# Optimization experiments

Hardware: AMD Instinct MI355X
Metric: run time of the kernel (lower is better)

Reference implementation:

```python
import jax, jax.numpy as jnp
import numpy as np

N = 100000   # nodes
E = 1600000  # edges (avg degree 16)
D = 64       # feature dim
LN_EPS = 1e-5


def setup_inputs() -> dict:
    key = jax.random.key(0)
    ks = jax.random.split(key, 12)
    s = 1.0 / np.sqrt(D)
    x = jax.random.normal(ks[0], (N, D), dtype=jnp.float32)
    edge_index = jax.random.randint(ks[1], (2, E), 0, N, dtype=jnp.int32)
    routing_factor = jax.random.uniform(ks[2], (E,), dtype=jnp.float32)
    return {
        "x": x,
        "edge_index": edge_index,
        "routing_factor": routing_factor,
        "W_phys": jax.random.normal(ks[3], (D, D), dtype=jnp.float32) * s,
        "W_neur": jax.random.normal(ks[4], (D, D), dtype=jnp.float32) * s,
        "att_w": jax.random.normal(ks[5], (2 * D,), dtype=jnp.float32) * s,
        "channel_fusion": jnp.float32(0.5),
        "mlp_w1": jax.random.normal(ks[6], (2 * D, D), dtype=jnp.float32) * s,
        "mlp_b1": jnp.zeros((2 * D,), dtype=jnp.float32),
        "mlp_w2": jax.random.normal(ks[7], (D, 2 * D), dtype=jnp.float32) / np.sqrt(2 * D),
        "mlp_b2": jnp.zeros((D,), dtype=jnp.float32),
        "ln1_g": jnp.ones((D,), dtype=jnp.float32),
        "ln1_b": jnp.zeros((D,), dtype=jnp.float32),
        "ln2_g": jnp.ones((D,), dtype=jnp.float32),
        "ln2_b": jnp.zeros((D,), dtype=jnp.float32),
    }


def _layernorm(h, g, b):
    mu = jnp.mean(h, axis=-1, keepdims=True)
    var = jnp.var(h, axis=-1, keepdims=True)
    return (h - mu) * jax.lax.rsqrt(var + LN_EPS) * g + b


def reference(x, edge_index, routing_factor, W_phys, W_neur, att_w,
              channel_fusion, mlp_w1, mlp_b1, mlp_w2, mlp_b2,
              ln1_g, ln1_b, ln2_g, ln2_b):
    src, dst = edge_index[0], edge_index[1]
    x_src = x[src]  # [E, D]
    # att(cat([x_src, x_dst])) == x_src @ w[:D] + x_dst @ w[D:]
    att_scores = x_src @ att_w[:D] + x[dst] @ att_w[D:]  # [E]
    # segment softmax over destination nodes (equivalent to per-node loop)
    seg_max = jax.ops.segment_max(att_scores, dst, num_segments=N)
    e = jnp.exp(att_scores - seg_max[dst])
    denom = jax.ops.segment_sum(e, dst, num_segments=N)
    att = e / denom[dst]  # [E]
    # dual-channel messages (dropout inactive at eval)
    phys = routing_factor[:, None] * (x_src @ W_phys.T)
    neur = x_src @ W_neur.T
    alpha = jax.nn.sigmoid(channel_fusion)
    messages = att[:, None] * (alpha * phys + (1.0 - alpha) * neur)  # [E, D]
    out = jax.ops.segment_sum(messages, dst, num_segments=N)  # [N, D]
    h = _layernorm(jax.nn.gelu(out, approximate=False) + x, ln1_g, ln1_b)
    m = jax.nn.gelu(h @ mlp_w1.T + mlp_b1, approximate=False) @ mlp_w2.T + mlp_b2
    return _layernorm(m + h, ln2_g, ln2_b)
```

## Files before the change

kernel.cpp:

```cpp
#include <hip/hip_runtime.h>
#include <math.h>

#define NN 100000
#define NE 1600000
#define DD 64
#define NBUK 782
#define TILE 2048
#define NTB ((NE + TILE - 1) / TILE)
#define BSTRIDE 3072
#define SCAP 3072

typedef __attribute__((ext_vector_type(8))) short short8;
typedef __attribute__((ext_vector_type(4))) float f32x4;
typedef __attribute__((ext_vector_type(4))) _Float16 h4;
typedef __attribute__((ext_vector_type(2))) _Float16 f16x2;

__device__ __forceinline__ float gelu_exact(float v) {
    return 0.5f * v * (1.0f + erff(v * 0.7071067811865475f));
}

__device__ __forceinline__ unsigned short f2bf(float f) {
    unsigned u = __float_as_uint(f);
    return (unsigned short)((u + 0x7FFFu + ((u >> 16) & 1u)) >> 16);
}
__device__ __forceinline__ float bf2f(unsigned short h) {
    return __uint_as_float((unsigned)h << 16);
}
__device__ __forceinline__ void split8v(float4 x0, float4 x1, short8& hi, short8& lo) {
    float v[8] = {x0.x, x0.y, x0.z, x0.w, x1.x, x1.y, x1.z, x1.w};
    #pragma unroll
    for (int i = 0; i < 8; ++i) {
        unsigned short h = f2bf(v[i]);
        hi[i] = (short)h;
        lo[i] = (short)f2bf(v[i] - bf2f(h));
    }
}
__device__ __forceinline__ void lds_frag(const float* g, int row, int u0, int s,
                                         short8& hi, short8& lo) {
    float4 p0 = *(const float4*)&g[row * 64 + ((u0 ^ s) << 2)];
    float4 p1 = *(const float4*)&g[row * 64 + (((u0 + 1) ^ s) << 2)];
    split8v(p0, p1, hi, lo);
}

__device__ __forceinline__ f16x2 as_f16x2(unsigned int u) {
    union { unsigned int x; f16x2 h; } c; c.x = u; return c.h;
}
__device__ __forceinline__ unsigned short h_as_us(_Float16 h) {
    union { _Float16 h; unsigned short u; } c; c.h = h; return c.u;
}
__device__ __forceinline__ float us_as_f(unsigned short u) {
    union { unsigned short u; _Float16 h; } c; c.u = u; return (float)c.h;
}

__global__ __launch_bounds__(256) void k01(
    const float* __restrict__ Wp, const float* __restrict__ Wn,
    const float* __restrict__ w1, const float* __restrict__ w2,
    const float* __restrict__ cf,
    unsigned short* __restrict__ wh, unsigned short* __restrict__ wl,
    const float* __restrict__ x, const float* __restrict__ attw,
    float* __restrict__ es1, _Float16* __restrict__ xh)
{
    int bid = blockIdx.x;
    if (bid < 96) {
        int t = bid * 256 + threadIdx.x;
        float alpha = 1.0f / (1.0f + __expf(-cf[0]));
        float beta  = 1.0f - alpha;
        float v;
        if (t < 8192) {
            int d = t >> 7, k = t & 127;
            v = (k < 64) ? alpha * Wp[d * 64 + k] : beta * Wn[d * 64 + (k - 64)];
        } else if (t < 16384) {
            v = w1[t - 8192];
        } else {
            v = w2[t - 16384];
        }
        unsigned short h = f2bf(v);
        wh[t] = h;
        wl[t] = f2bf(v - bf2f(h));
    } else {
        int n = (bid - 96) * 256 + threadIdx.x;
        if (n >= NN) return;
        const float4* x4 = (const float4*)(x + (size_t)n * DD);
        float a = 0.f;
        #pragma unroll
        for (int i = 0; i < DD/4; ++i) {
            float4 v = x4[i];
            a += v.x*attw[4*i+0] + v.y*attw[4*i+1] + v.z*attw[4*i+2] + v.w*attw[4*i+3];
            h4 hv = {(_Float16)v.x, (_Float16)v.y, (_Float16)v.z, (_Float16)v.w};
            *(h4*)(xh + (size_t)n * DD + 4*i) = hv;
        }
        es1[n] = __expf(a);
    }
}

__global__ __launch_bounds__(1024) void ks_bscan(
    const int* __restrict__ bcount, int* __restrict__ bbase)
{
    __shared__ int sa[1024], sb[1024];
    int t = threadIdx.x;
    int v = (t < NBUK) ? bcount[t] : 0;
    sa[t] = v;
    __syncthreads();
    int* s = sa; int* d = sb;
    #pragma unroll
    for (int o = 1; o < 1024; o <<= 1) {
        d[t] = s[t] + ((t >= o) ? s[t - o] : 0);
        __syncthreads();
        int* tmp = s; s = d; d = tmp;
    }
    if (t < NBUK) bbase[t] = s[t] - v;
    if (t == 0) bbase[NBUK] = NE;
}

__global__ __launch_bounds__(256) void kscat1(
    const int* __restrict__ ei, const float* __restrict__ rf,
    const float* __restrict__ es1,
    int* __restrict__ bcount, uint2* __restrict__ tmp)
{
    __shared__ int hist[NBUK];
    __shared__ int gbase[NBUK];
    for (int i = threadIdx.x; i < NBUK; i += 256) hist[i] = 0;
    __syncthreads();
    int base = blockIdx.x * TILE;
    int end  = min(base + TILE, NE);
    for (int e = base + threadIdx.x; e < end; e += 256)
        atomicAdd(&hist[ei[NE + e] >> 7], 1);
    __syncthreads();
    for (int i = threadIdx.x; i < NBUK; i += 256) {
        int c = hist[i];
        gbase[i] = c ? (i * BSTRIDE + atomicAdd(bcount + i, c)) : 0;
        hist[i] = 0;
    }
    __syncthreads();
    for (int e = base + threadIdx.x; e < end; e += 256) {
        int src = ei[e];
        int dst = ei[NE + e];
        float es = es1[src];
        float ef = es * rf[e];
        unsigned packed = (unsigned)h_as_us((_Float16)es)
                        | ((unsigned)h_as_us((_Float16)ef) << 16);
        int b = dst >> 7;
        int t = atomicAdd(&hist[b], 1);
        tmp[gbase[b] + t] =
            make_uint2((unsigned)src | ((unsigned)(dst & 127) << 17), packed);
    }
}

__global__ __launch_bounds__(256) void kscat2(
    const uint2* __restrict__ tmp, const int* __restrict__ bcount,
    const int* __restrict__ bbase,
    int* __restrict__ off, uint2* __restrict__ sorted)
{
    __shared__ int hist[128], scn[128], tick[128];
    __shared__ uint2 obuf[SCAP];
    int b   = blockIdx.x;
    int tid = threadIdx.x;
    int si = b * BSTRIDE;
    int so = bbase[b];
    int m  = bcount[b];

    if (tid < 128) { hist[tid] = 0; tick[tid] = 0; }
    __syncthreads();

    for (int i = tid; i < m; i += 256)
        atomicAdd(&hist[tmp[si + i].x >> 17], 1);
    __syncthreads();

    if (tid < 128) scn[tid] = hist[tid];
    __syncthreads();
    #pragma unroll
    for (int o = 1; o < 128; o <<= 1) {
        int v = (tid < 128 && tid >= o) ? scn[tid - o] : 0;
        __syncthreads();
        if (tid < 128) scn[tid] += v;
        __syncthreads();
    }

    int nb0 = b * 128;
    if (tid < 128 && nb0 + tid < NN) off[nb0 + tid] = so + scn[tid] - hist[tid];
    if (b == NBUK - 1 && tid == 0) off[NN] = NE;
    __syncthreads();

    for (int i = tid; i < m; i += 256) {
        uint2 pr = tmp[si + i];
        int l = pr.x >> 17;
        int t = atomicAdd(&tick[l], 1);
        int lp = (scn[l] - hist[l]) + t;
        uint2 val = make_uint2(pr.x & 0x1FFFFu, pr.y);
        if (lp < SCAP) obuf[lp] = val;
        else sorted[so + lp] = val;
    }
    __syncthreads();
    int mm = min(m, SCAP);
    for (int i = tid; i < mm; i += 256)
        sorted[so + i] = obuf[i];
}

__global__ __launch_bounds__(256) void k4a_agg(
    const uint2* __restrict__ sorted, const int* __restrict__ off,
    const _Float16* __restrict__ xh, float* __restrict__ uv)
{
    int lane = threadIdx.x & 63;
    int n = blockIdx.x * 4 + (threadIdx.x >> 6);
    int r0 = __builtin_amdgcn_readfirstlane(off[n]);
    int r1 = __builtin_amdgcn_readfirstlane(off[n + 1]);
    const unsigned short* xs = (const unsigned short*)xh;

    float den = 0.f, u = 0.f, v = 0.f;
    const unsigned ONES = 0x3C003C00u;
    int j = r0;
    for (; j + 8 <= r1; j += 8) {
        uint2 p[8];
        #pragma unroll
        for (int t = 0; t < 8; ++t) p[t] = sorted[j + t];
        unsigned xv[4];
        #pragma unroll
        for (int q = 0; q < 4; ++q) {
            unsigned a0 = xs[(size_t)p[2*q].x   * DD + lane];
            unsigned a1 = xs[(size_t)p[2*q+1].x * DD + lane];
            xv[q] = a0 | (a1 << 16);
        }
        #pragma unroll
        for (int q = 0; q < 4; ++q) {
            unsigned y0 = p[2*q].y, y1 = p[2*q+1].y;
            unsigned e2 = (y0 & 0xFFFFu) | (y1 << 16);
            unsigned f2 = (y0 >> 16) | (y1 & 0xFFFF0000u);
            v   = __builtin_amdgcn_fdot2(as_f16x2(xv[q]), as_f16x2(e2), v, false);
            u   = __builtin_amdgcn_fdot2(as_f16x2(xv[q]), as_f16x2(f2), u, false);
            den = __builtin_amdgcn_fdot2(as_f16x2(e2), as_f16x2(ONES), den, false);
        }
    }
    for (; j + 2 <= r1; j += 2) {
        uint2 p0 = sorted[j], p1 = sorted[j + 1];
        unsigned a0 = xs[(size_t)p0.x * DD + lane];
        unsigned a1 = xs[(size_t)p1.x * DD + lane];
        unsigned xv = a0 | (a1 << 16);
        unsigned e2 = (p0.y & 0xFFFFu) | (p1.y << 16);
        unsigned f2 = (p0.y >> 16) | (p1.y & 0xFFFF0000u);
        v   = __builtin_amdgcn_fdot2(as_f16x2(xv), as_f16x2(e2), v, false);
        u   = __builtin_amdgcn_fdot2(as_f16x2(xv), as_f16x2(f2), u, false);
        den = __builtin_amdgcn_fdot2(as_f16x2(e2), as_f16x2(ONES), den, false);
    }
    if (j < r1) {
        uint2 p0 = sorted[j];
        float xvf = us_as_f((unsigned short)xs[(size_t)p0.x * DD + lane]);
        float e = us_as_f((unsigned short)(p0.y & 0xFFFFu));
        float f = us_as_f((unsigned short)(p0.y >> 16));
        den += e; v += e * xvf; u += f * xvf;
    }
    float inv = (r1 > r0) ? 1.f / den : 0.f;
    uv[(size_t)n * 128 + lane]      = u * inv;
    uv[(size_t)n * 128 + 64 + lane] = v * inv;
}

__global__ __launch_bounds__(512, 4) void k4b5(
    const float* __restrict__ uv,
    const unsigned short* __restrict__ wh, const unsigned short* __restrict__ wl,
    const float* __restrict__ x,
    const float* __restrict__ g1, const float* __restrict__ be1,
    const float* __restrict__ bb1, const float* __restrict__ bb2,
    const float* __restrict__ g2, const float* __restrict__ be2,
    float* __restrict__ out)
{
    __shared__ unsigned short WH[8192], WL[8192];
    __shared__ unsigned short W2H[4096], W2L[4096];
    __shared__ float Gt[8][1024];

    int tid  = threadIdx.x;
    int lane = tid & 63;
    int wv   = tid >> 6;
    int quad = lane >> 4, l16 = lane & 15;
    int s7   = l16 & 7;
    int nb = blockIdx.x * 128 + wv * 16;
    float* gt = Gt[wv];

    const float4* arow4 = (const float4*)(uv + (size_t)min(nb + l16, NN - 1) * 128);
    float4 av[8];
    #pragma unroll
    for (int ks = 0; ks < 4; ++ks) {
        av[2*ks]   = arow4[ks*8 + quad*2];
        av[2*ks+1] = arow4[ks*8 + quad*2 + 1];
    }
    float xr[4][4];
    #pragma unroll
    for (int r = 0; r < 4; ++r) {
        size_t nld = (size_t)min(nb + quad*4 + r, NN - 1) * 64;
        #pragma unroll
        for (int nt = 0; nt < 4; ++nt) xr[r][nt] = x[nld + nt*16 + l16];
    }

    #pragma unroll
    for (int k = 0; k < 2; ++k) {
        int i = tid + k*512;
        int row = i >> 4, u = i & 15;
        int up = u ^ (row & 7);
        *(short8*)&WH[row*128 + up*8] = *(const short8*)&wh[i*8];
        *(short8*)&WL[row*128 + up*8] = *(const short8*)&wl[i*8];
    }
    __syncthreads();

    f32x4 acc0[4] = {};
    #pragma unroll
    for (int ks = 0; ks < 4; ++ks) {
        short8 ah, al;
        split8v(av[2*ks], av[2*ks+1], ah, al);
        int u0 = 4*ks + quad;
        #pragma unroll
        for (int nt = 0; nt < 4; ++nt) {
            int wo = (nt*16 + l16)*128 + (u0 ^ s7)*8;
            short8 bh = *(const short8*)&WH[wo];
            short8 bl = *(const short8*)&WL[wo];
            acc0[nt] = __builtin_amdgcn_mfma_f32_16x16x32_bf16(ah, bh, acc0[nt], 0, 0, 0);
            acc0[nt] = __builtin_amdgcn_mfma_f32_16x16x32_bf16(al, bh, acc0[nt], 0, 0, 0);
            acc0[nt] = __builtin_amdgcn_mfma_f32_16x16x32_bf16(ah, bl, acc0[nt], 0, 0, 0);
        }
    }

    float hn[4][4];
    #pragma unroll
    for (int r = 0; r < 4; ++r) {
        float hv[4];
        #pragma unroll
        for (int nt = 0; nt < 4; ++nt)
            hv[nt] = gelu_exact(acc0[nt][r]) + xr[r][nt];
        float s = hv[0] + hv[1] + hv[2] + hv[3];
        #pragma unroll
        for (int o = 1; o < 16; o <<= 1) s += __shfl_xor(s, o);
        float mu = s * (1.0f/64.0f);
        float q = 0.f;
        #pragma unroll
        for (int nt = 0; nt < 4; ++nt) { float t = hv[nt] - mu; q += t*t; }
        #pragma unroll
        for (int o = 1; o < 16; o <<= 1) q += __shfl_xor(q, o);
        float rs = rsqrtf(q * (1.0f/64.0f) + 1e-5f);
        int row = quad*4 + r;
        #pragma unroll
        for (int nt = 0; nt < 4; ++nt) {
            int c = nt*16 + l16;
            float h = (hv[nt] - mu) * rs * g1[c] + be1[c];
            hn[r][nt] = h;
            int u = c >> 2;
            gt[row*64 + ((u ^ (row & 7)) << 2) + (c & 3)] = h;
        }
    }
    __syncthreads();

    #pragma unroll
    for (int k = 0; k < 2; ++k) {
        int i = tid + k*512;
        int row = i >> 3, u = i & 7;
        int up = u ^ (row & 7);
        *(short8*)&WH[row*64 + up*8] = *(const short8*)&wh[8192 + i*8];
        *(short8*)&WL[row*64 + up*8] = *(const short8*)&wl[8192 + i*8];
    }
    {
        int row = tid >> 3, u = tid & 7;
        int up = u ^ (row & 7);
        *(short8*)&W2H[row*64 + up*8] = *(const short8*)&wh[16384 + row*128 + u*8];
        *(short8*)&W2L[row*64 + up*8] = *(const short8*)&wl[16384 + row*128 + u*8];
    }
    __syncthreads();

    short8 ah1[2], al1[2];
    #pragma unroll
    for (int ks = 0; ks < 2; ++ks)
        lds_frag(gt, l16, 8*ks + 2*quad, s7, ah1[ks], al1[ks]);

    f32x4 acc2[4] = {};
    #pragma unroll
    for (int half = 0; half < 2; ++half) {
        f32x4 a1[4] = {};
        #pragma unroll
        for (int ks = 0; ks < 2; ++ks) {
            int u0 = 4*ks + quad;
            #pragma unroll
            for (int t = 0; t < 4; ++t) {
                int row = half*64 + t*16 + l16;
                int wo = row*64 + ((u0 ^ s7))*8;
                short8 bh = *(const short8*)&WH[wo];
                short8 bl = *(const short8*)&WL[wo];
                a1[t] = __builtin_amdgcn_mfma_f32_16x16x32_bf16(ah1[ks], bh, a1[t], 0, 0, 0);
                a1[t] = __builtin_amdgcn_mfma_f32_16x16x32_bf16(al1[ks], bh, a1[t], 0, 0, 0);
                a1[t] = __builtin_amdgcn_mfma_f32_16x16x32_bf16(ah1[ks], bl, a1[t], 0, 0, 0);
            }
        }
        #pragma unroll
        for (int t = 0; t < 4; ++t) {
            float b1v = bb1[half*64 + t*16 + l16];
            #pragma unroll
            for (int r = 0; r < 4; ++r) {
                int row = quad*4 + r;
                int c = t*16 + l16;
                int u = c >> 2;
                gt[row*64 + ((u ^ (row & 7)) << 2) + (c & 3)] = gelu_exact(a1[t][r] + b1v);
            }
        }
        #pragma unroll
        for (int ks2 = 0; ks2 < 2; ++ks2) {
            short8 ah2, al2;
            lds_frag(gt, l16, 8*ks2 + 2*quad, s7, ah2, al2);
            int u0 = 4*ks2 + quad;
            #pragma unroll
            for (int nt2 = 0; nt2 < 4; ++nt2) {
                int wo = (nt2*16 + l16)*64 + (u0 ^ s7)*8;
                short8 bh = *(const short8*)&W2H[wo];
                short8 bl = *(const short8*)&W2L[wo];
                acc2[nt2] = __builtin_amdgcn_mfma_f32_16x16x32_bf16(ah2, bh, acc2[nt2], 0, 0, 0);
                acc2[nt2] = __builtin_amdgcn_mfma_f32_16x16x32_bf16(al2, bh, acc2[nt2], 0, 0, 0);
                acc2[nt2] = __builtin_amdgcn_mfma_f32_16x16x32_bf16(ah2, bl, acc2[nt2], 0, 0, 0);
            }
        }
        if (half == 0) {
            __syncthreads();
            int row = tid >> 3, u = tid & 7;
            int up = u ^ (row & 7);
            *(short8*)&W2H[row*64 + up*8] = *(const short8*)&wh[16384 + row*128 + 64 + u*8];
            *(short8*)&W2L[row*64 + up*8] = *(const short8*)&wl[16384 + row*128 + 64 + u*8];
            __syncthreads();
        }
    }

    #pragma unroll
    for (int r = 0; r < 4; ++r) {
        int n = nb + quad * 4 + r;
        float mv[4];
        #pragma unroll
        for (int nt = 0; nt < 4; ++nt)
            mv[nt] = acc2[nt][r] + hn[r][nt] + bb2[nt*16 + l16];
        float s = mv[0] + mv[1] + mv[2] + mv[3];
        #pragma unroll
        for (int o = 1; o < 16; o <<= 1) s += __shfl_xor(s, o);
        float mu = s * (1.0f/64.0f);
        float q = 0.f;
        #pragma unroll
        for (int nt = 0; nt < 4; ++nt) { float t = mv[nt] - mu; q += t*t; }
        #pragma unroll
        for (int o = 1; o < 16; o <<= 1) q += __shfl_xor(q, o);
        float rs = rsqrtf(q * (1.0f/64.0f) + 1e-5f);
        if (n < NN) {
            #pragma unroll
            for (int nt = 0; nt < 4; ++nt) {
                int c = nt*16 + l16;
                out[(size_t)n * 64 + c] = (mv[nt] - mu) * rs * g2[c] + be2[c];
            }
        }
    }
}

extern "C" void kernel_launch(void* const* d_in, const int* in_sizes, int n_in,
                              void* d_out, int out_size, void* d_ws, size_t ws_size,
                              hipStream_t stream) {
    const float* x    = (const float*)d_in[0];
    const int*   ei   = (const int*)d_in[1];
    const float* rf   = (const float*)d_in[2];
    const float* Wp   = (const float*)d_in[3];
    const float* Wn   = (const float*)d_in[4];
    const float* attw = (const float*)d_in[5];
    const float* cf   = (const float*)d_in[6];
    const float* w1   = (const float*)d_in[7];
    const float* b1   = (const float*)d_in[8];
    const float* w2   = (const float*)d_in[9];
    const float* b2   = (const float*)d_in[10];
    const float* g1   = (const float*)d_in[11];
    const float* be1  = (const float*)d_in[12];
    const float* g2   = (const float*)d_in[13];
    const float* be2  = (const float*)d_in[14];
    float* out = (float*)d_out;

    float* ws = (float*)d_ws;
    float*  es1    = ws;
    float*  uv     = es1 + NN;
    unsigned short* wh = (unsigned short*)(uv + (size_t)NN * 128);
    unsigned short* wl = wh + 24576;
    uint2*  sorted = (uint2*)(wl + 24576);
    int*    off    = (int*)(sorted + NE);
    int*    bcount = off + NN + 1;
    int*    bbase  = bcount + NBUK;
    uintptr_t xp = ((uintptr_t)(bbase + NBUK + 1) + 15) & ~(uintptr_t)15;
    _Float16* xh = (_Float16*)xp;
    uint2*  tmp    = (uint2*)uv;

    hipMemsetAsync(bcount, 0, NBUK * sizeof(int), stream);

    int k01grid = 96 + (NN + 255) / 256;
    k01       <<<k01grid, 256, 0, stream>>>(Wp, Wn, w1, w2, cf, wh, wl, x, attw, es1, xh);
    kscat1    <<<NTB, 256, 0, stream>>>(ei, rf, es1, bcount, tmp);
    ks_bscan  <<<1, 1024, 0, stream>>>(bcount, bbase);
    kscat2    <<<NBUK, 256, 0, stream>>>(tmp, bcount, bbase, off, sorted);
    k4a_agg   <<<NN/4, 256, 0, stream>>>(sorted, off, xh, uv);
    k4b5      <<<(NN+127)/128, 512, 0, stream>>>(uv, wh, wl, x, g1, be1, b1, b2, g2, be2, out);
}
```

Baseline: 306.0 us.

## Fuse edge bucketing scatter into front kernel and defer es1 gather to second pass

The first-pass edge scatter no longer depends on es1, so it is merged into the weight-prep/x-conversion kernel and runs concurrently with it, removing one launch and one dependency. The es1 lookup and fp16 packing move to kscat2, which carries the raw routing factor in the temp buffer instead. The tile size grows from 2048 to 8192 edges per block, and the scatter loop is unrolled by 4 to batch loads. The larger tile means fewer, longer-running blocks and fewer global bucket atomics. The es1 gather now happens in bucket order, which may change its locality.

After: 263.3 us. -13.9%, faster.

```diff
diff --git a/kernel.cpp b/kernel.cpp
--- a/kernel.cpp
+++ b/kernel.cpp
@@ -5,8 +5,10 @@
 #define NE 1600000
 #define DD 64
 #define NBUK 782
-#define TILE 2048
+#define TILE 8192
 #define NTB ((NE + TILE - 1) / TILE)
+#define NWB 96
+#define NPB ((NN + 255) / 256)
 #define BSTRIDE 3072
 #define SCAP 3072
 
@@ -52,7 +54,9 @@
     union { unsigned short u; _Float16 h; } c; c.u = u; return (float)c.h;
 }
 
-__global__ __launch_bounds__(256) void k01(
+__global__ __launch_bounds__(256) void kfront(
+    const int* __restrict__ ei, const float* __restrict__ rf,
+    int* __restrict__ bcount, uint2* __restrict__ tmp,
     const float* __restrict__ Wp, const float* __restrict__ Wn,
     const float* __restrict__ w1, const float* __restrict__ w2,
     const float* __restrict__ cf,
@@ -60,9 +64,50 @@
     const float* __restrict__ x, const float* __restrict__ attw,
     float* __restrict__ es1, _Float16* __restrict__ xh)
 {
+    __shared__ int hist[NBUK];
+    __shared__ int gbase[NBUK];
     int bid = blockIdx.x;
-    if (bid < 96) {
-        int t = bid * 256 + threadIdx.x;
+    int tid = threadIdx.x;
+
+    if (bid < NTB) {
+        for (int i = tid; i < NBUK; i += 256) hist[i] = 0;
+        __syncthreads();
+        int base = bid * TILE;
+        int end  = min(base + TILE, NE);
+        for (int e = base + tid; e < end; e += 256)
+            atomicAdd(&hist[ei[NE + e] >> 7], 1);
+        __syncthreads();
+        for (int i = tid; i < NBUK; i += 256) {
+            int c = hist[i];
+            gbase[i] = c ? (i * BSTRIDE + atomicAdd(bcount + i, c)) : 0;
+            hist[i] = 0;
+        }
+        __syncthreads();
+        for (int e0 = base + tid; e0 < end; e0 += 256 * 4) {
+            int srcs[4], dsts[4]; unsigned rfs[4];
+            #pragma unroll
+            for (int q = 0; q < 4; ++q) {
+                int e = e0 + q * 256;
+                if (e < end) {
+                    srcs[q] = ei[e];
+                    dsts[q] = ei[NE + e];
+                    rfs[q]  = __float_as_uint(rf[e]);
+                }
+            }
+            #pragma unroll
+            for (int q = 0; q < 4; ++q) {
+                int e = e0 + q * 256;
+                if (e < end) {
+                    int b = dsts[q] >> 7;
+                    int t = atomicAdd(&hist[b], 1);
+                    tmp[gbase[b] + t] = make_uint2(
+                        (unsigned)srcs[q] | ((unsigned)(dsts[q] & 127) << 17),
+                        rfs[q]);
+                }
+            }
+        }
+    } else if (bid < NTB + NWB) {
+        int t = (bid - NTB) * 256 + tid;
         float alpha = 1.0f / (1.0f + __expf(-cf[0]));
         float beta  = 1.0f - alpha;
         float v;
@@ -78,7 +123,7 @@
         wh[t] = h;
         wl[t] = f2bf(v - bf2f(h));
     } else {
-        int n = (bid - 96) * 256 + threadIdx.x;
+        int n = (bid - NTB - NWB) * 256 + tid;
         if (n >= NN) return;
         const float4* x4 = (const float4*)(x + (size_t)n * DD);
         float a = 0.f;
@@ -112,43 +157,9 @@
     if (t == 0) bbase[NBUK] = NE;
 }
 
-__global__ __launch_bounds__(256) void kscat1(
-    const int* __restrict__ ei, const float* __restrict__ rf,
-    const float* __restrict__ es1,
-    int* __restrict__ bcount, uint2* __restrict__ tmp)
-{
-    __shared__ int hist[NBUK];
-    __shared__ int gbase[NBUK];
-    for (int i = threadIdx.x; i < NBUK; i += 256) hist[i] = 0;
-    __syncthreads();
-    int base = blockIdx.x * TILE;
-    int end  = min(base + TILE, NE);
-    for (int e = base + threadIdx.x; e < end; e += 256)
-        atomicAdd(&hist[ei[NE + e] >> 7], 1);
-    __syncthreads();
-    for (int i = threadIdx.x; i < NBUK; i += 256) {
-        int c = hist[i];
-        gbase[i] = c ? (i * BSTRIDE + atomicAdd(bcount + i, c)) : 0;
-        hist[i] = 0;
-    }
-    __syncthreads();
-    for (int e = base + threadIdx.x; e < end; e += 256) {
-        int src = ei[e];
-        int dst = ei[NE + e];
-        float es = es1[src];
-        float ef = es * rf[e];
-        unsigned packed = (unsigned)h_as_us((_Float16)es)
-                        | ((unsigned)h_as_us((_Float16)ef) << 16);
-        int b = dst >> 7;
-        int t = atomicAdd(&hist[b], 1);
-        tmp[gbase[b] + t] =
-            make_uint2((unsigned)src | ((unsigned)(dst & 127) << 17), packed);
-    }
-}
-
 __global__ __launch_bounds__(256) void kscat2(
     const uint2* __restrict__ tmp, const int* __restrict__ bcount,
-    const int* __restrict__ bbase,
+    const int* __restrict__ bbase, const float* __restrict__ es1,
     int* __restrict__ off, uint2* __restrict__ sorted)
 {
     __shared__ int hist[128], scn[128], tick[128];
@@ -183,10 +194,15 @@
 
     for (int i = tid; i < m; i += 256) {
         uint2 pr = tmp[si + i];
-        int l = pr.x >> 17;
+        int l   = pr.x >> 17;
+        int src = pr.x & 0x1FFFF;
+        float es = es1[src];
+        float ef = es * __uint_as_float(pr.y);
+        unsigned packed = (unsigned)h_as_us((_Float16)es)
+                        | ((unsigned)h_as_us((_Float16)ef) << 16);
         int t = atomicAdd(&tick[l], 1);
         int lp = (scn[l] - hist[l]) + t;
-        uint2 val = make_uint2(pr.x & 0x1FFFFu, pr.y);
+        uint2 val = make_uint2((unsigned)src, packed);
         if (lp < SCAP) obuf[lp] = val;
         else sorted[so + lp] = val;
     }
@@ -482,11 +498,10 @@
 
     hipMemsetAsync(bcount, 0, NBUK * sizeof(int), stream);
 
-    int k01grid = 96 + (NN + 255) / 256;
-    k01       <<<k01grid, 256, 0, stream>>>(Wp, Wn, w1, w2, cf, wh, wl, x, attw, es1, xh);
-    kscat1    <<<NTB, 256, 0, stream>>>(ei, rf, es1, bcount, tmp);
+    kfront    <<<NTB + NWB + NPB, 256, 0, stream>>>(ei, rf, bcount, tmp,
+                 Wp, Wn, w1, w2, cf, wh, wl, x, attw, es1, xh);
     ks_bscan  <<<1, 1024, 0, stream>>>(bcount, bbase);
-    kscat2    <<<NBUK, 256, 0, stream>>>(tmp, bcount, bbase, off, sorted);
+    kscat2    <<<NBUK, 256, 0, stream>>>(tmp, bcount, bbase, es1, off, sorted);
     k4a_agg   <<<NN/4, 256, 0, stream>>>(sorted, off, xh, uv);
     k4b5      <<<(NN+127)/128, 512, 0, stream>>>(uv, wh, wl, x, g1, be1, b1, b2, g2, be2, out);
 }
```
